# Kernel optimization log

Hardware: AMD Instinct MI355X
Metric: run time of the kernel (lower is better)

## Reference

```python
import jax, jax.numpy as jnp
import numpy as np

N = 1_600_000          # total points across all polylines
NUM_SEG = 100_000      # number of polylines (segments for scatter_max)
C_IN = 64
C_OUT = 64
NEG_SLOPE = 0.01       # F.leaky_relu default


def setup_inputs() -> dict:
    key = jax.random.key(0)
    k1, k2, k3, k4 = jax.random.split(key, 4)
    features = jax.random.normal(k1, (N, C_IN), dtype=jnp.float32)
    W = jax.random.normal(k2, (C_OUT, C_IN), dtype=jnp.float32) * (1.0 / np.sqrt(C_IN))
    b = jax.random.normal(k3, (C_OUT,), dtype=jnp.float32) * 0.01
    agg_indices = jax.random.randint(k4, (N,), 0, NUM_SEG, dtype=jnp.int32)
    return {"features": features, "W": W, "b": b, "agg_indices": agg_indices}


def reference(features, W, b, agg_indices):
    # fc: Linear(in_channels, out_channels)  -> [N, C_OUT]
    h = features @ W.T + b
    # leaky_relu (default negative_slope=0.01)
    h = jnp.where(h >= 0, h, NEG_SLOPE * h)
    # scatter_max over segments (dim=0): [NUM_SEG, C_OUT]
    agg = jax.ops.segment_max(h, agg_indices, num_segments=NUM_SEG)
    # guard against empty segments (-inf from segment_max); torch_scatter leaves them 0
    agg = jnp.where(jnp.isfinite(agg), agg, 0.0)
    # gather-broadcast and concat -> [N, 2*C_OUT]
    out = jnp.concatenate([h, agg[agg_indices]], axis=-1)
    return out, agg
```

## Files before the change

### kernel.cpp

```cpp
#include <hip/hip_runtime.h>
#include <stdint.h>

#define C 64
#define CAP 64

typedef __attribute__((ext_vector_type(8))) short short8v;
typedef __attribute__((ext_vector_type(4))) float f32x4;

static __device__ __forceinline__ short f2bf(float f) {
    unsigned u = __float_as_uint(f);
    unsigned r = (u + 0x7FFFu + ((u >> 16) & 1u)) >> 16;
    return (short)r;
}

static __device__ __forceinline__ short8v cvt8(f32x4 lo, f32x4 hi) {
    short8v v;
    v[0] = f2bf(lo[0]); v[1] = f2bf(lo[1]); v[2] = f2bf(lo[2]); v[3] = f2bf(lo[3]);
    v[4] = f2bf(hi[0]); v[5] = f2bf(hi[1]); v[6] = f2bf(hi[2]); v[7] = f2bf(hi[3]);
    return v;
}

#define LOADA(t, L)                                                          \
    {                                                                        \
        const float* a0_ = feat + ((size_t)(t) * 32 + r) * C + q * 8;        \
        const float* a1_ = a0_ + 16 * C;                                     \
        L[0] = __builtin_nontemporal_load((const f32x4*)(a0_));              \
        L[1] = __builtin_nontemporal_load((const f32x4*)(a0_ + 4));          \
        L[2] = __builtin_nontemporal_load((const f32x4*)(a0_ + 32));         \
        L[3] = __builtin_nontemporal_load((const f32x4*)(a0_ + 36));         \
        L[4] = __builtin_nontemporal_load((const f32x4*)(a1_));              \
        L[5] = __builtin_nontemporal_load((const f32x4*)(a1_ + 4));          \
        L[6] = __builtin_nontemporal_load((const f32x4*)(a1_ + 32));         \
        L[7] = __builtin_nontemporal_load((const f32x4*)(a1_ + 36));         \
    }

__global__ __launch_bounds__(256) void k_gemm_fill(
    const float* __restrict__ feat, const float* __restrict__ W,
    const float* __restrict__ b, const int* __restrict__ idx,
    float* __restrict__ out, unsigned int* __restrict__ bucket, int N)
{
    const int lane = threadIdx.x & 63;
    const int gw   = blockIdx.x * (blockDim.x >> 6) + (threadIdx.x >> 6);
    const int nw   = gridDim.x * (blockDim.x >> 6);
    const int r    = lane & 15;
    const int q    = lane >> 4;

    short8v wf[4][2];
#pragma unroll
    for (int ct = 0; ct < 4; ++ct)
#pragma unroll
        for (int kh = 0; kh < 2; ++kh) {
            const float* src = W + (size_t)(ct * 16 + r) * C + kh * 32 + q * 8;
            wf[ct][kh] = cvt8(*(const f32x4*)src, *(const f32x4*)(src + 4));
        }
    float bias[4];
#pragma unroll
    for (int ct = 0; ct < 4; ++ct) bias[ct] = b[ct * 16 + r];

    const f32x4 zero = {0.f, 0.f, 0.f, 0.f};
    const int nTiles = N >> 5;

    f32x4 cur[8], nxt[8];
    int t = gw;
    if (t < nTiles) LOADA(t, cur);

    for (; t < nTiles; t += nw) {
        const int tn    = t + nw;
        const int rowid = t * 32 + lane;
        const int seg   = (lane < 32) ? idx[rowid] : 0;

        if (tn < nTiles) LOADA(tn, nxt);

        if (lane < 32) {
            unsigned int old = atomicAdd(&bucket[(size_t)seg * CAP], 1u);
            if (old < CAP - 1)
                bucket[(size_t)seg * CAP + 1 + old] = (unsigned int)rowid;
        }

        short8v A0k0 = cvt8(cur[0], cur[1]), A0k1 = cvt8(cur[2], cur[3]);
        short8v A1k0 = cvt8(cur[4], cur[5]), A1k1 = cvt8(cur[6], cur[7]);

        f32x4 d0[4], d1[4];
#pragma unroll
        for (int ct = 0; ct < 4; ++ct) {
            d0[ct] = __builtin_amdgcn_mfma_f32_16x16x32_bf16(A0k0, wf[ct][0], zero, 0, 0, 0);
            d0[ct] = __builtin_amdgcn_mfma_f32_16x16x32_bf16(A0k1, wf[ct][1], d0[ct], 0, 0, 0);
            d1[ct] = __builtin_amdgcn_mfma_f32_16x16x32_bf16(A1k0, wf[ct][0], zero, 0, 0, 0);
            d1[ct] = __builtin_amdgcn_mfma_f32_16x16x32_bf16(A1k1, wf[ct][1], d1[ct], 0, 0, 0);
        }

        const size_t row0 = (size_t)t * 32 + q * 4;
#pragma unroll
        for (int ct = 0; ct < 4; ++ct)
#pragma unroll
            for (int j = 0; j < 4; ++j) {
                float v0 = d0[ct][j] + bias[ct];
                v0 = fmaxf(v0, 0.01f * v0);
                __builtin_nontemporal_store(v0, &out[(row0 + j) * (2 * C) + ct * 16 + r]);
                float v1 = d1[ct][j] + bias[ct];
                v1 = fmaxf(v1, 0.01f * v1);
                __builtin_nontemporal_store(v1, &out[(row0 + 16 + j) * (2 * C) + ct * 16 + r]);
            }

#pragma unroll
        for (int i = 0; i < 8; ++i) cur[i] = nxt[i];
    }
}

__global__ __launch_bounds__(256) void k_reduce_scatter(
    float* __restrict__ out, unsigned int* __restrict__ bucket, int nseg)
{
    const int lane = threadIdx.x & 63;
    const int seg  = blockIdx.x * (blockDim.x >> 6) + (threadIdx.x >> 6);
    if (seg >= nseg) return;
    const int cq = lane >> 4;
    const int cc = (lane & 15) * 4;

    unsigned int* brow = bucket + (size_t)seg * CAP;
    const unsigned int v = brow[lane];
    int cnt = __shfl((int)v, 0, 64);
    if (cnt > CAP - 1) cnt = CAP - 1;

    const float ninf = -__builtin_inff();
    f32x4 acc = {ninf, ninf, ninf, ninf};

    const int ng = (cnt + 3) >> 2;
    for (int g = 0; g < ng; ++g) {
        int s    = 4 * g + cq;
        int slot = (s < cnt) ? (1 + s) : 1;
        int row  = __shfl((int)v, slot, 64);
        const float* src = out + (size_t)row * (2 * C) + cc;
        f32x4 hv = __builtin_nontemporal_load((const f32x4*)src);
        acc[0] = fmaxf(acc[0], hv[0]);
        acc[1] = fmaxf(acc[1], hv[1]);
        acc[2] = fmaxf(acc[2], hv[2]);
        acc[3] = fmaxf(acc[3], hv[3]);
    }

#pragma unroll
    for (int j = 0; j < 4; ++j) {
        float o = __shfl_xor(acc[j], 16, 64);
        acc[j] = fmaxf(acc[j], o);
        o = __shfl_xor(acc[j], 32, 64);
        acc[j] = fmaxf(acc[j], o);
    }

    if (cnt == 0) { acc[0] = 0.f; acc[1] = 0.f; acc[2] = 0.f; acc[3] = 0.f; }

    if (lane < 16)
        *(f32x4*)((float*)brow + cc) = acc;

    for (int g = 0; g < ng; ++g) {
        int s    = 4 * g + cq;
        int slot = (s < cnt) ? (1 + s) : 1;
        int row  = __shfl((int)v, slot, 64);
        float* dst = out + (size_t)row * (2 * C) + C + cc;
        __builtin_nontemporal_store(acc, (f32x4*)dst);
    }
}

extern "C" void kernel_launch(void* const* d_in, const int* in_sizes, int n_in,
                              void* d_out, int out_size, void* d_ws, size_t ws_size,
                              hipStream_t stream)
{
    (void)n_in; (void)d_ws; (void)ws_size;
    const float* feat = (const float*)d_in[0];
    const float* W    = (const float*)d_in[1];
    const float* b    = (const float*)d_in[2];
    const int*   idx  = (const int*)d_in[3];
    float* out = (float*)d_out;

    const int N    = in_sizes[0] / C;
    const int nseg = (out_size - N * 2 * C) / C;

    float* aggOut = out + (size_t)N * 2 * C;
    unsigned int* bucket = (unsigned int*)aggOut;

    hipMemsetAsync(aggOut, 0, (size_t)nseg * CAP * sizeof(unsigned int), stream);

    k_gemm_fill<<<2048, 256, 0, stream>>>(feat, W, b, idx, out, bucket, N);
    k_reduce_scatter<<<(nseg + 3) / 4, 256, 0, stream>>>(out, bucket, nseg);
}
```

Measured before the change: 432.2 us.

## Split segment reduce from broadcast and batch row loads in reduce loop

Segment reduction now only computes per-segment max and writes agg; a new streaming gather kernel then writes agg[idx[n]] into the second half of each output row in sequential order, replacing scattered per-row stores. The reduce loop issues up to four row loads before doing the max, to raise memory-level parallelism. This costs an extra launch and an extra read of idx and agg, but turns random writes into coalesced ones.

```diff
diff --git a/kernel.cpp b/kernel.cpp
--- a/kernel.cpp
+++ b/kernel.cpp
@@ -107,8 +107,8 @@
     }
 }
 
-__global__ __launch_bounds__(256) void k_reduce_scatter(
-    float* __restrict__ out, unsigned int* __restrict__ bucket, int nseg)
+__global__ __launch_bounds__(256) void k_reduce(
+    const float* __restrict__ h, unsigned int* __restrict__ bucket, int nseg)
 {
     const int lane = threadIdx.x & 63;
     const int seg  = blockIdx.x * (blockDim.x >> 6) + (threadIdx.x >> 6);
@@ -125,16 +125,28 @@
     f32x4 acc = {ninf, ninf, ninf, ninf};
 
     const int ng = (cnt + 3) >> 2;
-    for (int g = 0; g < ng; ++g) {
-        int s    = 4 * g + cq;
-        int slot = (s < cnt) ? (1 + s) : 1;
-        int row  = __shfl((int)v, slot, 64);
-        const float* src = out + (size_t)row * (2 * C) + cc;
-        f32x4 hv = __builtin_nontemporal_load((const f32x4*)src);
-        acc[0] = fmaxf(acc[0], hv[0]);
-        acc[1] = fmaxf(acc[1], hv[1]);
-        acc[2] = fmaxf(acc[2], hv[2]);
-        acc[3] = fmaxf(acc[3], hv[3]);
+    for (int base = 0; base < ng; base += 4) {
+        int nb = ng - base; if (nb > 4) nb = 4;
+        f32x4 hv[4];
+#pragma unroll
+        for (int u = 0; u < 4; ++u) {
+            if (u < nb) {
+                int sx   = 4 * (base + u) + cq;
+                int slot = (sx < cnt) ? (1 + sx) : 1;
+                int row  = __shfl((int)v, slot, 64);
+                hv[u] = __builtin_nontemporal_load(
+                    (const f32x4*)(h + (size_t)row * (2 * C) + cc));
+            }
+        }
+#pragma unroll
+        for (int u = 0; u < 4; ++u) {
+            if (u < nb) {
+                acc[0] = fmaxf(acc[0], hv[u][0]);
+                acc[1] = fmaxf(acc[1], hv[u][1]);
+                acc[2] = fmaxf(acc[2], hv[u][2]);
+                acc[3] = fmaxf(acc[3], hv[u][3]);
+            }
+        }
     }
 
 #pragma unroll
@@ -149,13 +161,20 @@
 
     if (lane < 16)
         *(f32x4*)((float*)brow + cc) = acc;
-
-    for (int g = 0; g < ng; ++g) {
-        int s    = 4 * g + cq;
-        int slot = (s < cnt) ? (1 + s) : 1;
-        int row  = __shfl((int)v, slot, 64);
-        float* dst = out + (size_t)row * (2 * C) + C + cc;
-        __builtin_nontemporal_store(acc, (f32x4*)dst);
+}
+
+__global__ __launch_bounds__(256) void k_gather(
+    const f32x4* __restrict__ agg, const int* __restrict__ idx,
+    f32x4* __restrict__ out4, long long total)
+{
+    long long i      = (long long)blockIdx.x * blockDim.x + threadIdx.x;
+    long long stride = (long long)gridDim.x * blockDim.x;
+    for (; i < total; i += stride) {
+        int n  = (int)(i >> 4);
+        int qq = (int)(i & 15);
+        int seg = idx[n];
+        f32x4 a = agg[(size_t)seg * 16 + qq];
+        __builtin_nontemporal_store(a, &out4[(size_t)n * 32 + 16 + qq]);
     }
 }
 
@@ -179,5 +198,7 @@
     hipMemsetAsync(aggOut, 0, (size_t)nseg * CAP * sizeof(unsigned int), stream);
 
     k_gemm_fill<<<2048, 256, 0, stream>>>(feat, W, b, idx, out, bucket, N);
-    k_reduce_scatter<<<(nseg + 3) / 4, 256, 0, stream>>>(out, bucket, nseg);
-}
+    k_reduce<<<(nseg + 3) / 4, 256, 0, stream>>>(out, bucket, nseg);
+    k_gather<<<4096, 256, 0, stream>>>((const f32x4*)aggOut, idx,
+                                       (f32x4*)out, (long long)N * 16);
+}
```

After: 463.4 us. +7.2%, slower.
